# Kernel tuning notes

Measured on AMD Instinct MI355X. Metric: run time of the kernel, lower is better.

## Reference

```python
import jax, jax.numpy as jnp
import numpy as np

D = 512       # d_model
H = 8         # n_heads
HD = D // H   # head_dim = 64
BS = 64       # block_size
B = 1
S = 8192
NB = S // BS  # 128 blocks
THRESH = 0.3


def setup_inputs() -> dict:
    key = jax.random.key(0)
    ks = jax.random.split(key, 6)
    sc = 0.02
    return {
        "x": jax.random.normal(ks[0], (B, S, D), jnp.float32),
        "w_qkv": (jax.random.normal(ks[1], (D, 3 * D)) * sc).astype(jnp.float32),
        "b_qkv": jnp.zeros((3 * D,), jnp.float32),
        "w_out": (jax.random.normal(ks[2], (D, D)) * sc).astype(jnp.float32),
        "b_out": jnp.zeros((D,), jnp.float32),
        "w_r1": (jax.random.normal(ks[3], (D, 128)) * sc).astype(jnp.float32),
        "b_r1": jnp.zeros((128,), jnp.float32),
        "w_r2": (jax.random.normal(ks[4], (128, 1)) * sc).astype(jnp.float32),
        "b_r2": jnp.full((1,), 0.5, jnp.float32),  # sigmoid(~0.5)>0.3 -> non-degenerate mask
    }


def reference(x, w_qkv, b_qkv, w_out, b_out, w_r1, b_r1, w_r2, b_r2):
    Bx, Sx, Dx = x.shape
    qkv = (x @ w_qkv + b_qkv).reshape(Bx, Sx, 3, H, HD)
    q = jnp.transpose(qkv[:, :, 0], (0, 2, 1, 3))  # [B,H,S,HD]
    k = jnp.transpose(qkv[:, :, 1], (0, 2, 1, 3))
    v = jnp.transpose(qkv[:, :, 2], (0, 2, 1, 3))

    # --- router: per-block importance from mean-pooled q block (d_model features) ---
    qb = q.reshape(Bx, H, NB, BS, HD)
    rep = jnp.transpose(qb.mean(axis=3), (0, 2, 1, 3)).reshape(Bx, NB, Dx)  # [B,NB,D]
    imp = jax.nn.sigmoid(jax.nn.relu(rep @ w_r1 + b_r1) @ w_r2 + b_r2)[..., 0]  # [B,NB]
    keep = (imp.mean(axis=0) >= THRESH).astype(x.dtype)  # [NB], shared across batch (torch uses batch-mean)

    kb = k.reshape(Bx, H, NB, BS, HD)
    vb = v.reshape(Bx, H, NB, BS, HD)
    tri = jnp.triu(jnp.ones((BS, BS), bool), 1)  # strict upper triangle within diagonal block
    jidx = jnp.arange(NB)
    scale = 1.0 / np.sqrt(HD)

    def step(carry, i):
        q_i = jax.lax.dynamic_slice_in_dim(q, i * BS, BS, axis=2)        # [B,H,BSq,HD]
        s = jnp.einsum('bhqd,bhjkd->bhqjk', q_i, kb) * scale             # [B,H,BSq,NB,BSk]
        causal = (jidx == i)[None, :, None] & tri[:, None, :]            # [BSq,NB,BSk]
        s = jnp.where(causal[None, None], -jnp.inf, s)
        p = jax.nn.softmax(s, axis=-1)                                   # softmax PER key-block (as in torch loop)
        wj = keep * keep[i]                                              # block pair gate [NB]
        o = jnp.einsum('bhqjk,j,bhjkd->bhqd', p, wj, vb)                 # sum of gated per-block contributions
        return carry, o

    _, outs = jax.lax.scan(step, None, jnp.arange(NB))                   # [NB,B,H,BSq,HD]
    attn = jnp.transpose(outs, (1, 2, 0, 3, 4)).reshape(Bx, H, Sx, HD)
    attn = jnp.transpose(attn, (0, 2, 1, 3)).reshape(Bx, Sx, Dx)
    return attn @ w_out + b_out
```

## Files before the change

### kernel.cpp

```cpp
#include <hip/hip_runtime.h>

typedef unsigned short u16;
typedef unsigned int u32;
typedef __attribute__((ext_vector_type(8))) short short8;
typedef __attribute__((ext_vector_type(4))) short short4v;
typedef __attribute__((ext_vector_type(4))) float f32x4;
typedef __attribute__((ext_vector_type(4))) float float4v;
typedef __attribute__((ext_vector_type(2))) u32 u32x2;
typedef __attribute__((ext_vector_type(4))) u32 u32x4;

#define S_LEN 8192
#define NHEAD 8
#define NBLK  128
#define SCALE_C 0.18033688011112042f

__device__ __forceinline__ u16 f2b(float f) {
    union { float f; unsigned u; } v; v.f = f;
    unsigned r = v.u + 0x7FFFu + ((v.u >> 16) & 1u);
    return (u16)(r >> 16);
}
__device__ __forceinline__ float b2f(u16 b) {
    union { float f; unsigned u; } v; v.u = ((unsigned)b) << 16; return v.f;
}
__device__ __forceinline__ u32 cvt_pk_bf16(float lo, float hi) {
    u32 r;
    asm("v_cvt_pk_bf16_f32 %0, %1, %2" : "=v"(r) : "v"(lo), "v"(hi));
    return r;
}
__device__ __forceinline__ void pl16swap(u32& a, u32& b) {
    u32x2 r = __builtin_amdgcn_permlane16_swap(a, b, false, false);
    a = r[0]; b = r[1];
}
__device__ __forceinline__ void pl32swap(u32& a, u32& b) {
    u32x2 r = __builtin_amdgcn_permlane32_swap(a, b, false, false);
    a = r[0]; b = r[1];
}
__device__ __forceinline__ int swz(int row, int colByte) {
    return row * 128 + (colByte ^ ((row & 7) << 4));
}
__device__ __forceinline__ void gload_lds(const void* g, void* l) {
    __builtin_amdgcn_global_load_lds(
        (const __attribute__((address_space(1))) void*)g,
        (__attribute__((address_space(3))) void*)l, 16, 0, 0);
}

__global__ __launch_bounds__(256) void cvt_x_kernel(const float* __restrict__ x, u16* __restrict__ xb) {
    int idx = blockIdx.x * 256 + threadIdx.x;
    float4v v = *((const float4v*)x + idx);
    short4v o;
    #pragma unroll
    for (int r = 0; r < 4; ++r) o[r] = (short)f2b(v[r]);
    *((short4v*)xb + idx) = o;
}

__global__ __launch_bounds__(256) void cvt_T_kernel(const float* __restrict__ w, u16* __restrict__ wt, int C) {
    int idx = blockIdx.x * 256 + threadIdx.x;
    int r = idx & 511, cc = idx >> 9;
    wt[idx] = f2b(w[(size_t)r * C + cc]);
}

__global__ __launch_bounds__(256) void sum4_kernel(const u16* __restrict__ a0, const u16* __restrict__ a1,
                                                   const u16* __restrict__ a2, const u16* __restrict__ a3,
                                                   int n, u16* __restrict__ outb) {
    int idx = blockIdx.x * 256 + threadIdx.x;
    short8 v0 = ((const short8*)a0)[idx];
    short8 v1 = ((const short8*)a1)[idx];
    float s[8];
    #pragma unroll
    for (int e = 0; e < 8; ++e) s[e] = b2f((u16)v0[e]) + b2f((u16)v1[e]);
    if (n == 4) {
        short8 v2 = ((const short8*)a2)[idx];
        short8 v3 = ((const short8*)a3)[idx];
        #pragma unroll
        for (int e = 0; e < 8; ++e) s[e] += b2f((u16)v2[e]) + b2f((u16)v3[e]);
    }
    short8 o;
    #pragma unroll
    for (int e = 0; e < 8; ++e) o[e] = (short)f2b(s[e]);
    ((short8*)outb)[idx] = o;
}

__device__ __forceinline__ void gemm128_core(const u16* __restrict__ A,
                                             const u16* __restrict__ Bt,
                                             int m0, int n0, char* As, char* Bs,
                                             f32x4 acc[4][4]) {
    const int tid = threadIdx.x;
    const int lane = tid & 63, wid = tid >> 6;
    const int q16 = lane >> 4, l16 = lane & 15;
    const int wm = wid >> 1, wn = wid & 1;
    #pragma unroll 1
    for (int kt = 0; kt < 8; ++kt) {
        const int k0 = kt * 64;
        __syncthreads();
        #pragma unroll
        for (int p = 0; p < 4; ++p) {
            int c = tid + p * 256;
            int row = c >> 3, colp = (c & 7) ^ (row & 7);
            gload_lds(A  + (size_t)(m0 + row) * 512 + k0 + colp * 8, As + (size_t)(wid * 64 + p * 256) * 16);
            gload_lds(Bt + (size_t)(n0 + row) * 512 + k0 + colp * 8, Bs + (size_t)(wid * 64 + p * 256) * 16);
        }
        __syncthreads();
        #pragma unroll
        for (int kk = 0; kk < 2; ++kk) {
            short8 a[4], b[4];
            #pragma unroll
            for (int t = 0; t < 4; ++t) {
                int arow = wm * 64 + t * 16 + l16;
                a[t] = *(const short8*)(As + swz(arow, kk * 64 + q16 * 16));
                int brow = wn * 64 + t * 16 + l16;
                b[t] = *(const short8*)(Bs + swz(brow, kk * 64 + q16 * 16));
            }
            #pragma unroll
            for (int mt = 0; mt < 4; ++mt)
                #pragma unroll
                for (int nt = 0; nt < 4; ++nt)
                    acc[mt][nt] = __builtin_amdgcn_mfma_f32_16x16x32_bf16(a[mt], b[nt], acc[mt][nt], 0, 0, 0);
        }
    }
}

__global__ __launch_bounds__(256) void qkv_gemm(const u16* __restrict__ xb, const u16* __restrict__ wqkvT,
                                                const float* __restrict__ bqkv,
                                                u16* __restrict__ qb, u16* __restrict__ kf, u16* __restrict__ vf) {
    __shared__ char smem[32768];
    f32x4 acc[4][4];
    #pragma unroll
    for (int a = 0; a < 4; ++a)
        #pragma unroll
        for (int b = 0; b < 4; ++b) acc[a][b] = (f32x4){0.f, 0.f, 0.f, 0.f};
    const int m0 = blockIdx.x * 128, n0 = blockIdx.y * 128;
    gemm128_core(xb, wqkvT, m0, n0, smem, smem + 16384, acc);

    const int lane = threadIdx.x & 63, wid = threadIdx.x >> 6;
    const int q16 = lane >> 4, l16 = lane & 15;
    const int wm = wid >> 1, wn = wid & 1;
    #pragma unroll
    for (int mt = 0; mt < 4; ++mt) {
        #pragma unroll
        for (int nt = 0; nt < 4; ++nt) {
            int n = n0 + wn * 64 + nt * 16 + l16;
            float bias = bqkv[n];
            int t = n >> 9, h = (n >> 6) & 7, d = n & 63;
            int sb = m0 + wm * 64 + mt * 16 + q16 * 4;
            f32x4 v = acc[mt][nt];
            if (t == 0) {
                #pragma unroll
                for (int r = 0; r < 4; ++r)
                    qb[(size_t)(h * S_LEN + sb + r) * 64 + d] = f2b((v[r] + bias) * SCALE_C);
            } else if (t == 1) {
                int j = sb >> 6, key = sb & 63;
                int n0k = key >> 4, c = d >> 5, q16k = (d >> 3) & 3, e = d & 7;
                int ub = (n0k * 2 + c) * 64 + q16k * 16 + (key & 15);
                u16* base = kf + (size_t)h * 524288 + (size_t)j * 4096 + e;
                #pragma unroll
                for (int r = 0; r < 4; ++r)
                    base[(ub + r) * 8] = f2b(v[r] + bias);
            } else {
                int j = sb >> 6, key = sb & 63;
                int dt = d >> 4, c = key >> 5, q16v = (key >> 3) & 3, e0 = key & 7;
                int u = (dt * 2 + c) * 64 + q16v * 16 + (d & 15);
                short4v pk;
                #pragma unroll
                for (int r = 0; r < 4; ++r) pk[r] = (short)f2b(v[r] + bias);
                *(short4v*)(vf + (size_t)h * 524288 + (size_t)j * 4096 + u * 8 + e0) = pk;
            }
        }
    }
}

__global__ __launch_bounds__(256) void out_gemm(const u16* __restrict__ a0, const u16* __restrict__ wotT,
                                                const float* __restrict__ bout, float* __restrict__ out) {
    __shared__ char smem[32768];
    f32x4 acc[4][4];
    #pragma unroll
    for (int a = 0; a < 4; ++a)
        #pragma unroll
        for (int b = 0; b < 4; ++b) acc[a][b] = (f32x4){0.f, 0.f, 0.f, 0.f};
    const int m0 = blockIdx.x * 128, n0 = blockIdx.y * 128;
    gemm128_core(a0, wotT, m0, n0, smem, smem + 16384, acc);

    const int lane = threadIdx.x & 63, wid = threadIdx.x >> 6;
    const int q16 = lane >> 4, l16 = lane & 15;
    const int wm = wid >> 1, wn = wid & 1;
    #pragma unroll
    for (int mt = 0; mt < 4; ++mt) {
        #pragma unroll
        for (int nt = 0; nt < 4; ++nt) {
            int n = n0 + wn * 64 + nt * 16 + l16;
            float bias = bout[n];
            int sb = m0 + wm * 64 + mt * 16 + q16 * 4;
            #pragma unroll
            for (int r = 0; r < 4; ++r)
                out[(size_t)(sb + r) * 512 + n] = acc[mt][nt][r] + bias;
        }
    }
}

__global__ __launch_bounds__(256) void router_kernel(const u16* __restrict__ qb,
                                                     const float* __restrict__ w_r1, const float* __restrict__ b_r1,
                                                     const float* __restrict__ w_r2, const float* __restrict__ b_r2,
                                                     float* __restrict__ keepf) {
    const int nb = blockIdx.x, tid = threadIdx.x;
    __shared__ float rep[512];
    __shared__ float h1[128];
    for (int dim = tid; dim < 512; dim += 256) {
        int h = dim >> 6, d = dim & 63;
        const u16* p = qb + (size_t)(h * S_LEN + nb * 64) * 64 + d;
        float s = 0.f;
        #pragma unroll 4
        for (int t = 0; t < 64; ++t) s += b2f(p[t * 64]);
        rep[dim] = s * (0.015625f / SCALE_C);
    }
    __syncthreads();
    if (tid < 128) {
        float a = b_r1[tid];
        for (int k = 0; k < 512; ++k) a += rep[k] * w_r1[k * 128 + tid];
        h1[tid] = fmaxf(a, 0.f);
    }
    __syncthreads();
    if (tid < 64) {
        float v = h1[tid] * w_r2[tid] + h1[tid + 64] * w_r2[tid + 64];
        #pragma unroll
        for (int off = 32; off; off >>= 1) v += __shfl_down(v, off);
        if (tid == 0) {
            float z = v + b_r2[0];
            keepf[nb] = (z >= -0.84729786f) ? 1.0f : 0.0f;
        }
    }
}

__global__ __launch_bounds__(256, 3) void attn_kernel(const u16* __restrict__ qb, const u16* __restrict__ kf,
                                                      const u16* __restrict__ vf, const float* __restrict__ keepf,
                                                      u16* __restrict__ a0, u16* __restrict__ a1,
                                                      u16* __restrict__ a2, u16* __restrict__ a3, int nj) {
    const int i = blockIdx.x, h = blockIdx.y, jh = blockIdx.z;
    const int j0 = jh * nj;
    u16* __restrict__ att = (jh == 0) ? a0 : (jh == 1) ? a1 : (jh == 2) ? a2 : a3;
    const int tid = threadIdx.x, lane = tid & 63, wid = tid >> 6;
    const int q16 = lane >> 4, l16 = lane & 15;
    __shared__ char smem[49152];

    short8 bq[2][2];
    #pragma unroll
    for (int qh = 0; qh < 2; ++qh) {
        const u16* qrow = qb + (size_t)(h * S_LEN + i * 128 + wid * 32 + qh * 16 + l16) * 64;
        bq[qh][0] = *(const short8*)(qrow + q16 * 8);
        bq[qh][1] = *(const short8*)(qrow + 32 + q16 * 8);
    }
    const int kq_s = __builtin_amdgcn_readfirstlane(i * 2 + (wid >> 1));
    const float keep_i = keepf[kq_s];
    const u32 kvbits = __builtin_bit_cast(u32, keepf[(j0 + lane) & 127]);
    const int qloc = (wid & 1) * 32 + l16;

    f32x4 o[2][4];
    #pragma unroll
    for (int qh = 0; qh < 2; ++qh)
        #pragma unroll
        for (int t = 0; t < 4; ++t) o[qh][t] = (f32x4){0.f, 0.f, 0.f, 0.f};

    const int lb = lane * 16;
    const int stoff = (wid * 128 + lane) * 8;
    const int ldw = wid * 2048;

    const u16* kst = kf + (size_t)h * 524288 + stoff + (size_t)j0 * 4096;
    const u16* vst = vf + (size_t)h * 524288 + stoff + (size_t)j0 * 4096;
    char *bA = smem, *bB = smem + 16384, *bC = smem + 32768;

    asm volatile("s_waitcnt vmcnt(0)" ::: "memory");

    auto STAGE = [&](char* dst) {
        gload_lds(kst,       dst + ldw);          gload_lds(kst + 512, dst + ldw + 1024);
        gload_lds(vst,       dst + 8192 + ldw);   gload_lds(vst + 512, dst + 8192 + ldw + 1024);
        kst += 4096; vst += 4096;
    };
    auto QK = [&](const char* Kc, f32x4 (&s)[2][4]) {
        __builtin_amdgcn_s_setprio(1);
        #pragma unroll
        for (int n0 = 0; n0 < 4; ++n0) {
            short8 ka0 = *(const short8*)(Kc + n0 * 2048 + lb);
            short8 ka1 = *(const short8*)(Kc + n0 * 2048 + 1024 + lb);
            #pragma unroll
            for (int qh = 0; qh < 2; ++qh) {
                f32x4 a = (f32x4){0.f, 0.f, 0.f, 0.f};
                a = __builtin_amdgcn_mfma_f32_16x16x32_bf16(ka0, bq[qh][0], a, 0, 0, 0);
                a = __builtin_amdgcn_mfma_f32_16x16x32_bf16(ka1, bq[qh][1], a, 0, 0, 0);
                s[qh][n0] = a;
            }
        }
        __builtin_amdgcn_s_setprio(0);
    };
    auto SMPV = [&](int jjl, const f32x4 (&s)[2][4], const char* Vc) {
        const float kj = __builtin_bit_cast(float, (u32)__builtin_amdgcn_readlane((int)kvbits, jjl));
        const float gj = keep_i * kj;
        const int j = j0 + jjl;
        short8 pb[2][2];
        #pragma unroll
        for (int qh = 0; qh < 2; ++qh) {
            f32x4 p4[4];
            #pragma unroll
            for (int n0 = 0; n0 < 4; ++n0)
                #pragma unroll
                for (int r = 0; r < 4; ++r)
                    p4[n0][r] = __builtin_amdgcn_exp2f(s[qh][n0][r]);
            if (j == kq_s) {
                const int qthis = qloc + qh * 16;
                #pragma unroll
                for (int n0 = 0; n0 < 4; ++n0)
                    #pragma unroll
                    for (int r = 0; r < 4; ++r)
                        if (n0 * 16 + q16 * 4 + r > qthis) p4[n0][r] = 0.f;
            }
            f32x4 sv = (p4[0] + p4[1]) + (p4[2] + p4[3]);
            float sum = (sv[0] + sv[1]) + (sv[2] + sv[3]);
            {
                u32 sa = __builtin_bit_cast(u32, sum), sb = sa;
                pl16swap(sa, sb);
                sum = __builtin_bit_cast(float, sa) + __builtin_bit_cast(float, sb);
                u32 sc = __builtin_bit_cast(u32, sum), sd = sc;
                pl32swap(sc, sd);
                sum = __builtin_bit_cast(float, sc) + __builtin_bit_cast(float, sd);
            }
            const float rinv = gj * __builtin_amdgcn_rcpf(sum);
            u32 dw[4][2];
            #pragma unroll
            for (int n0 = 0; n0 < 4; ++n0) {
                f32x4 t = p4[n0] * rinv;
                dw[n0][0] = cvt_pk_bf16(t[0], t[1]);
                dw[n0][1] = cvt_pk_bf16(t[2], t[3]);
            }
            #pragma unroll
            for (int kk = 0; kk < 2; ++kk) {
                u32 c0 = dw[2 * kk][0], d0 = dw[2 * kk + 1][0];
                pl32swap(c0, d0);
                pl16swap(c0, d0);
                u32 c1 = dw[2 * kk][1], d1 = dw[2 * kk + 1][1];
                pl32swap(c1, d1);
                pl16swap(c1, d1);
                u32x4 wv;
                wv[0] = c0; wv[1] = c1; wv[2] = d0; wv[3] = d1;
                pb[qh][kk] = __builtin_bit_cast(short8, wv);
            }
        }
        __builtin_amdgcn_s_setprio(1);
        #pragma unroll
        for (int dt = 0; dt < 4; ++dt) {
            short8 va0 = *(const short8*)(Vc + dt * 2048 + lb);
            short8 va1 = *(const short8*)(Vc + dt * 2048 + 1024 + lb);
            #pragma unroll
            for (int qh = 0; qh < 2; ++qh) {
                o[qh][dt] = __builtin_amdgcn_mfma_f32_16x16x32_bf16(va0, pb[qh][0], o[qh][dt], 0, 0, 0);
                o[qh][dt] = __builtin_amdgcn_mfma_f32_16x16x32_bf16(va1, pb[qh][1], o[qh][dt], 0, 0, 0);
            }
        }
        __builtin_amdgcn_s_setprio(0);
    };
    auto WAITBAR = [&]() {
        asm volatile("s_waitcnt vmcnt(0)" ::: "memory");
        __builtin_amdgcn_s_barrier();
        __builtin_amdgcn_sched_barrier(0);
    };
    auto ROT = [&]() { char* t = bA; bA = bB; bB = bC; bC = t; };

    STAGE(bA);
    STAGE(bB);
    asm volatile("s_waitcnt vmcnt(4)" ::: "memory");
    __builtin_amdgcn_s_barrier();

    f32x4 sA[2][4], sB[2][4];
    QK(bA, sA);

    for (int jj = 0; jj + 3 < nj; jj += 2) {
        WAITBAR();
        STAGE(bC);
        QK(bB, sB);
        SMPV(jj, sA, bA + 8192);
        ROT();
        WAITBAR();
        STAGE(bC);
        QK(bB, sA);
        SMPV(jj + 1, sB, bA + 8192);
        ROT();
    }
    WAITBAR();
    QK(bB, sB);
    SMPV(nj - 2, sA, bA + 8192);
    ROT();
    WAITBAR();
    SMPV(nj - 1, sB, bA + 8192);

    #pragma unroll
    for (int qh = 0; qh < 2; ++qh) {
        u16* obase = att + (size_t)(i * 128 + wid * 32 + qh * 16 + l16) * 512 + h * 64 + q16 * 4;
        #pragma unroll
        for (int dt = 0; dt < 4; ++dt) {
            u32x2 st;
            st[0] = cvt_pk_bf16(o[qh][dt][0], o[qh][dt][1]);
            st[1] = cvt_pk_bf16(o[qh][dt][2], o[qh][dt][3]);
            *(u32x2*)(obase + dt * 16) = st;
        }
    }
}

static const size_t OFF_WQKVT = 0;
static const size_t OFF_WOTT  = (size_t)2u << 20;
static const size_t OFF_KEEP  = ((size_t)2u << 20) + (512u << 10);
static const size_t OFF_QB    = (size_t)3u << 20;
static const size_t OFF_KF    = (size_t)11u << 20;
static const size_t OFF_VF    = (size_t)19u << 20;
static const size_t OFF_XB    = (size_t)27u << 20;
static const size_t OFF_P0    = (size_t)35u << 20;
static const size_t OFF_P1    = (size_t)43u << 20;
static const size_t OFF_P2    = (size_t)51u << 20;

extern "C" void kernel_launch(void* const* d_in, const int* in_sizes, int n_in,
                              void* d_out, int out_size, void* d_ws, size_t ws_size,
                              hipStream_t stream) {
    const float* x     = (const float*)d_in[0];
    const float* w_qkv = (const float*)d_in[1];
    const float* b_qkv = (const float*)d_in[2];
    const float* w_out = (const float*)d_in[3];
    const float* b_out = (const float*)d_in[4];
    const float* w_r1  = (const float*)d_in[5];
    const float* b_r1  = (const float*)d_in[6];
    const float* w_r2  = (const float*)d_in[7];
    const float* b_r2  = (const float*)d_in[8];
    float* out = (float*)d_out;
    char* ws = (char*)d_ws;
    u16* wqkvT  = (u16*)(ws + OFF_WQKVT);
    u16* wotT   = (u16*)(ws + OFF_WOTT);
    float* keepf = (float*)(ws + OFF_KEEP);
    u16* qb     = (u16*)(ws + OFF_QB);
    u16* kf     = (u16*)(ws + OFF_KF);
    u16* vf     = (u16*)(ws + OFF_VF);
    u16* xb     = (u16*)(ws + OFF_XB);
    u16* attnb  = (u16*)(ws + OFF_QB);

    const bool big = ws_size >= ((size_t)59u << 20) + 4096;
    const int njh = big ? 4 : 2;
    const int nj  = NBLK / njh;
    u16* a0 = (u16*)(ws + OFF_P0);
    u16* a1 = big ? (u16*)(ws + OFF_P1) : (u16*)(ws + OFF_XB);
    u16* a2 = big ? (u16*)(ws + OFF_P2) : a0;
    u16* a3 = big ? (u16*)(ws + OFF_XB) : a0;

    cvt_x_kernel<<<4096, 256, 0, stream>>>(x, xb);
    cvt_T_kernel<<<3072, 256, 0, stream>>>(w_qkv, wqkvT, 1536);
    cvt_T_kernel<<<1024, 256, 0, stream>>>(w_out, wotT, 512);
    qkv_gemm<<<dim3(64, 12), 256, 0, stream>>>(xb, wqkvT, b_qkv, qb, kf, vf);
    router_kernel<<<128, 256, 0, stream>>>(qb, w_r1, b_r1, w_r2, b_r2, keepf);
    attn_kernel<<<dim3(64, 8, njh), 256, 0, stream>>>(qb, kf, vf, keepf, a0, a1, a2, a3, nj);
    sum4_kernel<<<2048, 256, 0, stream>>>(a0, a1, a2, a3, njh, attnb);
    out_gemm<<<dim3(64, 4), 256, 0, stream>>>(attnb, wotT, b_out, out);
}
```

Measured before the change: 240.3 us.

## Split K/V staging buffers to cut LDS and raise attention occupancy

Replaces the triple-buffered combined K+V LDS ring (48 KB) with a double-buffered K ring and a triple-buffered V ring (40 KB). K is consumed one stage earlier than V, so it needs only two slots. The smaller LDS footprint lets launch bounds rise from 3 to 4 workgroups per CU to improve latency hiding. In exchange it lowers the per-thread register budget, which may cause spills, and the new buffer rotation must keep the K/V reuse ordering correct.

```diff
diff --git a/kernel.cpp b/kernel.cpp
--- a/kernel.cpp
+++ b/kernel.cpp
@@ -229,7 +229,7 @@
     }
 }
 
-__global__ __launch_bounds__(256, 3) void attn_kernel(const u16* __restrict__ qb, const u16* __restrict__ kf,
+__global__ __launch_bounds__(256, 4) void attn_kernel(const u16* __restrict__ qb, const u16* __restrict__ kf,
                                                       const u16* __restrict__ vf, const float* __restrict__ keepf,
                                                       u16* __restrict__ a0, u16* __restrict__ a1,
                                                       u16* __restrict__ a2, u16* __restrict__ a3, int nj) {
@@ -238,7 +238,7 @@
     u16* __restrict__ att = (jh == 0) ? a0 : (jh == 1) ? a1 : (jh == 2) ? a2 : a3;
     const int tid = threadIdx.x, lane = tid & 63, wid = tid >> 6;
     const int q16 = lane >> 4, l16 = lane & 15;
-    __shared__ char smem[49152];
+    __shared__ char smem[40960];
 
     short8 bq[2][2];
     #pragma unroll
@@ -264,13 +264,14 @@
 
     const u16* kst = kf + (size_t)h * 524288 + stoff + (size_t)j0 * 4096;
     const u16* vst = vf + (size_t)h * 524288 + stoff + (size_t)j0 * 4096;
-    char *bA = smem, *bB = smem + 16384, *bC = smem + 32768;
+    char *kRead = smem + 8192, *kStage = smem;
+    char *vPV = smem + 16384, *vNext = smem + 24576, *vStage = smem + 32768;
 
     asm volatile("s_waitcnt vmcnt(0)" ::: "memory");
 
-    auto STAGE = [&](char* dst) {
-        gload_lds(kst,       dst + ldw);          gload_lds(kst + 512, dst + ldw + 1024);
-        gload_lds(vst,       dst + 8192 + ldw);   gload_lds(vst + 512, dst + 8192 + ldw + 1024);
+    auto STAGE = [&](char* kdst, char* vdst) {
+        gload_lds(kst,       kdst + ldw);   gload_lds(kst + 512, kdst + ldw + 1024);
+        gload_lds(vst,       vdst + ldw);   gload_lds(vst + 512, vdst + ldw + 1024);
         kst += 4096; vst += 4096;
     };
     auto QK = [&](const char* Kc, f32x4 (&s)[2][4]) {
@@ -359,34 +360,37 @@
         __builtin_amdgcn_s_barrier();
         __builtin_amdgcn_sched_barrier(0);
     };
-    auto ROT = [&]() { char* t = bA; bA = bB; bB = bC; bC = t; };
-
-    STAGE(bA);
-    STAGE(bB);
+    auto ROT = [&]() {
+        char* t = kRead; kRead = kStage; kStage = t;
+        char* u = vPV; vPV = vNext; vNext = vStage; vStage = u;
+    };
+
+    STAGE(kStage, vPV);
+    STAGE(kRead, vNext);
     asm volatile("s_waitcnt vmcnt(4)" ::: "memory");
     __builtin_amdgcn_s_barrier();
 
     f32x4 sA[2][4], sB[2][4];
-    QK(bA, sA);
+    QK(kStage, sA);
 
     for (int jj = 0; jj + 3 < nj; jj += 2) {
         WAITBAR();
-        STAGE(bC);
-        QK(bB, sB);
-        SMPV(jj, sA, bA + 8192);
+        STAGE(kStage, vStage);
+        QK(kRead, sB);
+        SMPV(jj, sA, vPV);
         ROT();
         WAITBAR();
-        STAGE(bC);
-        QK(bB, sA);
-        SMPV(jj + 1, sB, bA + 8192);
+        STAGE(kStage, vStage);
+        QK(kRead, sA);
+        SMPV(jj + 1, sB, vPV);
         ROT();
     }
     WAITBAR();
-    QK(bB, sB);
-    SMPV(nj - 2, sA, bA + 8192);
+    QK(kRead, sB);
+    SMPV(nj - 2, sA, vPV);
     ROT();
     WAITBAR();
-    SMPV(nj - 1, sB, bA + 8192);
+    SMPV(nj - 1, sB, vPV);
 
     #pragma unroll
     for (int qh = 0; qh < 2; ++qh) {
```

Result: no change. 240.5 us (+0.1%).
